# Optimization experiments

Hardware: AMD Instinct MI355X
Metric: run time of the kernel (lower is better)

## Reference

```python
import jax, jax.numpy as jnp
import numpy as np


def setup_inputs() -> dict:
    key = jax.random.key(0)
    kq, kk, kv = jax.random.split(key, 3)
    n, m, d, v = 4096, 4096, 1024, 1024
    Q = jax.random.normal(kq, (n, d), dtype=jnp.float32)
    K = jax.random.normal(kk, (m, d), dtype=jnp.float32)
    V = jax.random.normal(kv, (m, v), dtype=jnp.float32)
    return {"Q": Q, "K": K, "V": V}


def reference(Q, K, V):
    d = K.shape[-1]
    scale = d ** (-0.5)
    logits = jnp.matmul(Q, K.T)                      # [n, m]
    # Faithful to source: softmax over dim=1 (keys), THEN scaled by d**-0.5
    scores = jax.nn.softmax(logits, axis=1) * scale  # [n, m]
    return jnp.matmul(scores, V)                     # [n, v]
```

## Files before the change

kernel.cpp:

```cpp
#include <hip/hip_runtime.h>
#include <hip/hip_bf16.h>

typedef _Float16 f16x8 __attribute__((ext_vector_type(8)));
typedef _Float16 f16x4 __attribute__((ext_vector_type(4)));
typedef float f32x4 __attribute__((ext_vector_type(4)));

__device__ __forceinline__ void async_ld16(_Float16* lds, const _Float16* g) {
    __builtin_amdgcn_global_load_lds(
        (const __attribute__((address_space(1))) void*)g,
        (__attribute__((address_space(3))) void*)lds, 16, 0, 0);
}

#define VMCNT(n) asm volatile("s_waitcnt vmcnt(" #n ")" ::: "memory")
#define LGKMCNT0 asm volatile("s_waitcnt lgkmcnt(0)" ::: "memory")
#define BAR() __builtin_amdgcn_s_barrier()

template <typename CT>
__global__ __launch_bounds__(512, 2) void gemm_bt256(
    const _Float16* __restrict__ A,
    const _Float16* __restrict__ B,
    CT* __restrict__ C,
    int M, int N, int K, int Ks)
{
    __shared__ _Float16 Asm[2][256 * 64];
    __shared__ _Float16 Bsm[2][256 * 64];

    const int tid  = threadIdx.x;
    const int w    = tid >> 6;
    const int lane = tid & 63;
    const int l16  = lane & 15;
    const int quad = lane >> 4;
    const int wm   = w >> 2;
    const int wn   = w & 3;

    const int gx = gridDim.x, gy = gridDim.y;
    const int total = gx * gy * (int)gridDim.z;
    int lid = (int)blockIdx.x + gx * ((int)blockIdx.y + gy * (int)blockIdx.z);
    int bx, by, bz;
    if (gx == 16 && gy == 16 && gridDim.z == 1) {
        const int xcd = lid & 7, i = lid >> 3;
        bx = (xcd & 1) * 8 + (i & 7);
        by = (xcd >> 1) * 4 + (i >> 3);
        bz = 0;
    } else {
        const int q = total >> 3, r = total & 7;
        const int xcd = lid & 7, i = lid >> 3;
        lid = (xcd < r ? xcd * (q + 1) : r * (q + 1) + (xcd - r) * q) + i;
        bx = lid % gx;
        by = (lid / gx) % gy;
        bz = lid / (gx * gy);
    }

    const int row0 = by * 256;
    const int col0 = bx * 256;

    const _Float16* Ab = A + (size_t)row0 * K + (size_t)bz * Ks;
    const _Float16* Bb = B + (size_t)col0 * K + (size_t)bz * Ks;

    const int lr = lane >> 3;
    const int lc = (lane & 7) ^ lr;
    const size_t soff  = (size_t)(w * 16 + lr) * K + lc * 8;
    const _Float16* pa = Ab + soff;
    const _Float16* pb = Bb + soff;
    const size_t jstep = (size_t)8 * K;
    const size_t hstep = (size_t)128 * K;

    auto STAGE = [&](_Float16* sm, const _Float16* gsrc, int h, int kcol) {
        _Float16* d = sm + h * 8192 + w * 1024;
        const _Float16* s = gsrc + (size_t)h * hstep + kcol;
        async_ld16(d,       s);
        async_ld16(d + 512, s + jstep);
    };

    const int abase = (wm * 16 + l16) * 64;
    const int bbase = (wn * 16 + l16) * 64;
    const int rs0   = ((quad)     ^ (l16 & 7)) * 8;
    const int rs1   = ((4 + quad) ^ (l16 & 7)) * 8;

#define READ_A(dst, msoff)                                                     \
    _Pragma("unroll")                                                          \
    for (int m_ = 0; m_ < 4; ++m_) {                                           \
        dst[m_][0] = *(const f16x8*)(abuf + (msoff) + m_ * 2048 + abase + rs0);\
        dst[m_][1] = *(const f16x8*)(abuf + (msoff) + m_ * 2048 + abase + rs1);\
    }
#define READ_B(dst, nsoff)                                                     \
    _Pragma("unroll")                                                          \
    for (int n_ = 0; n_ < 2; ++n_) {                                           \
        dst[n_][0] = *(const f16x8*)(bbuf + (nsoff) + n_ * 4096 + bbase + rs0);\
        dst[n_][1] = *(const f16x8*)(bbuf + (nsoff) + n_ * 4096 + bbase + rs1);\
    }
#define MFMA4x2(accrow, afrag, bfrag, bcol)                                    \
    _Pragma("unroll")                                                          \
    for (int m_ = 0; m_ < 4; ++m_)                                             \
      _Pragma("unroll")                                                        \
      for (int n_ = 0; n_ < 2; ++n_) {                                         \
        acc[(accrow) + m_][(bcol) + n_] =                                      \
            __builtin_amdgcn_mfma_f32_16x16x32_f16(                            \
                afrag[m_][0], bfrag[n_][0], acc[(accrow) + m_][(bcol) + n_],   \
                0, 0, 0);                                                      \
        acc[(accrow) + m_][(bcol) + n_] =                                      \
            __builtin_amdgcn_mfma_f32_16x16x32_f16(                            \
                afrag[m_][1], bfrag[n_][1], acc[(accrow) + m_][(bcol) + n_],   \
                0, 0, 0);                                                      \
      }

    f32x4 acc[8][4] = {};
    const int NT = Ks >> 6;

    STAGE(&Asm[0][0], pa, 0, 0);
    STAGE(&Bsm[0][0], pb, 0, 0);
    STAGE(&Bsm[0][0], pb, 1, 0);
    STAGE(&Asm[0][0], pa, 1, 0);
    if (NT > 1) {
        STAGE(&Asm[1][0], pa, 0, 64);
        STAGE(&Bsm[1][0], pb, 0, 64);
        STAGE(&Bsm[1][0], pb, 1, 64);
        VMCNT(6);
    } else {
        VMCNT(0);
    }
    BAR();

    for (int t = 0; t < NT; ++t) {
        const int buf = t & 1;
        const _Float16* abuf = &Asm[buf][0];
        const _Float16* bbuf = &Bsm[buf][0];
        _Float16* const acur = &Asm[buf][0];
        _Float16* const bcur = &Bsm[buf][0];
        _Float16* const anxt = &Asm[buf ^ 1][0];

        f16x8 alo[4][2], ahi[4][2], blo[2][2], bhi[2][2];

        READ_A(alo, 0);
        READ_B(blo, 0);
        if (t + 1 < NT) STAGE(anxt, pa, 1, (t + 1) * 64);
        BAR();
        LGKMCNT0;
        __builtin_amdgcn_s_setprio(1);
        MFMA4x2(0, alo, blo, 0);
        __builtin_amdgcn_s_setprio(0);
        BAR();

        READ_B(bhi, 8192);
        if (t + 2 < NT) STAGE(acur, pa, 0, (t + 2) * 64);
        BAR();
        LGKMCNT0;
        __builtin_amdgcn_s_setprio(1);
        MFMA4x2(0, alo, bhi, 2);
        __builtin_amdgcn_s_setprio(0);
        BAR();

        READ_A(ahi, 8192);
        if (t + 2 < NT) STAGE(bcur, pb, 0, (t + 2) * 64);
        BAR();
        LGKMCNT0;
        __builtin_amdgcn_s_setprio(1);
        MFMA4x2(4, ahi, bhi, 2);
        __builtin_amdgcn_s_setprio(0);
        BAR();

        if (t + 2 < NT) STAGE(bcur, pb, 1, (t + 2) * 64);
        BAR();
        __builtin_amdgcn_s_setprio(1);
        MFMA4x2(4, ahi, blo, 0);
        __builtin_amdgcn_s_setprio(0);
        if (t + 2 < NT) { VMCNT(6); } else { VMCNT(0); }
        BAR();
    }

    CT* Cb = C + (size_t)bz * ((size_t)M * N);
    #pragma unroll
    for (int i = 0; i < 8; ++i) {
        const int ms = i >> 2, m = i & 3;
        const int gr = row0 + ms * 128 + m * 32 + wm * 16 + quad * 4;
        #pragma unroll
        for (int j = 0; j < 4; ++j) {
            const int ns = j >> 1, nn = j & 1;
            const int gc = col0 + ns * 128 + nn * 64 + wn * 16 + l16;
            const f32x4 v = acc[i][j];
            #pragma unroll
            for (int e = 0; e < 4; ++e)
                Cb[(size_t)(gr + e) * N + gc] = (CT)v[e];
        }
    }
#undef READ_A
#undef READ_B
#undef MFMA4x2
}

__global__ __launch_bounds__(256) void gemm_bt(
    const _Float16* __restrict__ A,
    const _Float16* __restrict__ B,
    float* __restrict__ C,
    int M, int N, int K, int Ks)
{
    __shared__ _Float16 At[2][128 * 32];
    __shared__ _Float16 Bt[2][128 * 32];

    const int tid  = threadIdx.x;
    const int wave = tid >> 6;
    const int lane = tid & 63;

    int gx = gridDim.x, gy = gridDim.y;
    int bx = blockIdx.x, by = blockIdx.y;
    if (((gx & 7) == 0) && ((gy & 7) == 0)) {
        const int bid    = bx + gx * by;
        const int ntx    = gx >> 3;
        const int sid    = bid >> 6;
        const int within = bid & 63;
        const int sx = sid % ntx;
        const int sy = sid / ntx;
        bx = (sx << 3) + (within & 7);
        by = (sy << 3) + (within >> 3);
    }
    const int row0 = by * 128;
    const int col0 = bx * 128;

    const int wr = (wave >> 1) * 64;
    const int wc = (wave & 1) * 64;
    const int quad = lane >> 4;
    const int l16  = lane & 15;

    f32x4 acc[4][4] = {};

    const int srow  = lane >> 2;
    const int skoff = (lane & 3) * 8;
    const size_t K64 = (size_t)64 * K;

    const _Float16* Ab = A + (size_t)row0 * K + (size_t)blockIdx.z * Ks;
    const _Float16* Bb = B + (size_t)col0 * K + (size_t)blockIdx.z * Ks;
    float* Cb = C + (size_t)blockIdx.z * M * N;

    const _Float16* pa = Ab + (size_t)(wave * 16 + srow) * K + skoff;
    const _Float16* pb = Bb + (size_t)(wave * 16 + srow) * K + skoff;

    async_ld16(At[0] + wave * 512,       pa);
    async_ld16(At[0] + (wave + 4) * 512, pa + K64);
    async_ld16(Bt[0] + wave * 512,       pb);
    async_ld16(Bt[0] + (wave + 4) * 512, pb + K64);
    __syncthreads();

    int cur = 0;
    for (int k0 = 0; k0 < Ks; k0 += 32) {
        const int nxt = cur ^ 1;
        if (k0 + 32 < Ks) {
            const _Float16* qa = pa + k0 + 32;
            const _Float16* qb = pb + k0 + 32;
            async_ld16(At[nxt] + wave * 512,       qa);
            async_ld16(At[nxt] + (wave + 4) * 512, qa + K64);
            async_ld16(Bt[nxt] + wave * 512,       qb);
            async_ld16(Bt[nxt] + (wave + 4) * 512, qb + K64);
        }

        f16x8 af[4], bf[4];
        #pragma unroll
        for (int r = 0; r < 4; ++r)
            af[r] = *(const f16x8*)&At[cur][(wr + r * 16 + l16) * 32 + quad * 8];
        #pragma unroll
        for (int c = 0; c < 4; ++c)
            bf[c] = *(const f16x8*)&Bt[cur][(wc + c * 16 + l16) * 32 + quad * 8];

        #pragma unroll
        for (int r = 0; r < 4; ++r)
            #pragma unroll
            for (int c = 0; c < 4; ++c)
                acc[r][c] = __builtin_amdgcn_mfma_f32_16x16x32_f16(af[r], bf[c], acc[r][c], 0, 0, 0);

        __syncthreads();
        cur = nxt;
    }

    #pragma unroll
    for (int r = 0; r < 4; ++r) {
        const int growb = row0 + wr + r * 16 + quad * 4;
        #pragma unroll
        for (int c = 0; c < 4; ++c) {
            const int gcol = col0 + wc + c * 16 + l16;
            #pragma unroll
            for (int i = 0; i < 4; ++i)
                Cb[(size_t)(growb + i) * N + gcol] = acc[r][c][i];
        }
    }
}

__global__ __launch_bounds__(256) void softmax_rows(
    const float* __restrict__ S, _Float16* __restrict__ P, float scale)
{
    __shared__ float red[4];
    const int row = blockIdx.x;
    const int tid = threadIdx.x;
    const int wave = tid >> 6;
    const float4* Sr = (const float4*)(S + (size_t)row * 4096);

    float4 x[4];
    #pragma unroll
    for (int i = 0; i < 4; ++i) x[i] = Sr[tid + i * 256];

    float mx = -3.402823466e+38f;
    #pragma unroll
    for (int i = 0; i < 4; ++i)
        mx = fmaxf(mx, fmaxf(fmaxf(x[i].x, x[i].y), fmaxf(x[i].z, x[i].w)));
    #pragma unroll
    for (int off = 32; off > 0; off >>= 1) mx = fmaxf(mx, __shfl_down(mx, off));
    if ((tid & 63) == 0) red[wave] = mx;
    __syncthreads();
    mx = fmaxf(fmaxf(red[0], red[1]), fmaxf(red[2], red[3]));
    __syncthreads();

    float sum = 0.0f;
    #pragma unroll
    for (int i = 0; i < 4; ++i) {
        x[i].x = __expf(x[i].x - mx);
        x[i].y = __expf(x[i].y - mx);
        x[i].z = __expf(x[i].z - mx);
        x[i].w = __expf(x[i].w - mx);
        sum += x[i].x + x[i].y + x[i].z + x[i].w;
    }
    #pragma unroll
    for (int off = 32; off > 0; off >>= 1) sum += __shfl_down(sum, off);
    if ((tid & 63) == 0) red[wave] = sum;
    __syncthreads();
    sum = red[0] + red[1] + red[2] + red[3];

    const float inv = scale / sum;
    f16x4* Pr = (f16x4*)(P + (size_t)row * 4096);
    #pragma unroll
    for (int i = 0; i < 4; ++i) {
        f16x4 h;
        h.x = (_Float16)(x[i].x * inv);
        h.y = (_Float16)(x[i].y * inv);
        h.z = (_Float16)(x[i].z * inv);
        h.w = (_Float16)(x[i].w * inv);
        Pr[tid + i * 256] = h;
    }
}

__global__ __launch_bounds__(256) void prep(
    const float4* __restrict__ Qs, f16x4* __restrict__ Qh, int n4q,
    const float4* __restrict__ Ks, f16x4* __restrict__ Kh, int n4k,
    const float* __restrict__ V, _Float16* __restrict__ Vt, int rows, int cols)
{
    __shared__ float tile[32][33];
    if (blockIdx.y == 0) {
        int i = blockIdx.x * 256 + threadIdx.x;
        const int stride = gridDim.x * 256;
        const int tot = n4q + n4k;
        for (; i < tot; i += stride) {
            const float4* s = (i < n4q) ? (Qs + i) : (Ks + (i - n4q));
            f16x4* dst = (i < n4q) ? (Qh + i) : (Kh + (i - n4q));
            float4 v = *s;
            f16x4 h;
            h.x = (_Float16)v.x; h.y = (_Float16)v.y;
            h.z = (_Float16)v.z; h.w = (_Float16)v.w;
            *dst = h;
        }
    } else {
        const int cb = blockIdx.x & 31;
        const int rb = blockIdx.x >> 5;
        const int c0 = cb * 32;
        const int r0 = rb * 32;
        const int tx = threadIdx.x & 31;
        const int ty = threadIdx.x >> 5;
        #pragma unroll
        for (int i = 0; i < 4; ++i)
            tile[ty * 4 + i][tx] = V[(size_t)(r0 + ty * 4 + i) * cols + c0 + tx];
        __syncthreads();
        #pragma unroll
        for (int i = 0; i < 4; ++i)
            Vt[(size_t)(c0 + ty * 4 + i) * rows + r0 + tx] = (_Float16)tile[tx][ty * 4 + i];
    }
}

__global__ __launch_bounds__(256) void cvt2_f32_f16(
    const float4* __restrict__ a, f16x4* __restrict__ da, int n4a,
    const float4* __restrict__ b, f16x4* __restrict__ db, int n4b)
{
    int i = blockIdx.x * 256 + threadIdx.x;
    const int stride = gridDim.x * 256;
    const int tot = n4a + n4b;
    for (; i < tot; i += stride) {
        const float4* s = (i < n4a) ? (a + i) : (b + (i - n4a));
        f16x4* d = (i < n4a) ? (da + i) : (db + (i - n4a));
        float4 v = *s;
        f16x4 h;
        h.x = (_Float16)v.x; h.y = (_Float16)v.y;
        h.z = (_Float16)v.z; h.w = (_Float16)v.w;
        *d = h;
    }
}

__global__ __launch_bounds__(256) void transpose_cvt(
    const float* __restrict__ V, _Float16* __restrict__ Vt, int rows, int cols)
{
    __shared__ float tile[32][33];
    const int c0 = blockIdx.x * 32;
    const int r0 = blockIdx.y * 32;
    const int tx = threadIdx.x & 31;
    const int ty = threadIdx.x >> 5;
    #pragma unroll
    for (int i = 0; i < 4; ++i)
        tile[ty * 4 + i][tx] = V[(size_t)(r0 + ty * 4 + i) * cols + c0 + tx];
    __syncthreads();
    #pragma unroll
    for (int i = 0; i < 4; ++i)
        Vt[(size_t)(c0 + ty * 4 + i) * rows + r0 + tx] = (_Float16)tile[tx][ty * 4 + i];
}

__global__ __launch_bounds__(256) void reduce2(
    const float4* __restrict__ a, const float4* __restrict__ b,
    float4* __restrict__ o, int n4)
{
    int i = blockIdx.x * 256 + threadIdx.x;
    const int stride = gridDim.x * 256;
    for (; i < n4; i += stride) {
        float4 u = a[i], v = b[i];
        float4 w;
        w.x = u.x + v.x; w.y = u.y + v.y; w.z = u.z + v.z; w.w = u.w + v.w;
        o[i] = w;
    }
}

__global__ __launch_bounds__(256) void reduce4h(
    const f16x8* __restrict__ a, const f16x8* __restrict__ b,
    const f16x8* __restrict__ c, const f16x8* __restrict__ d,
    float4* __restrict__ o, int n8)
{
    int i = blockIdx.x * 256 + threadIdx.x;
    const int stride = gridDim.x * 256;
    for (; i < n8; i += stride) {
        f16x8 u = a[i], v = b[i], x = c[i], y = d[i];
        float s[8];
        #pragma unroll
        for (int e = 0; e < 8; ++e)
            s[e] = ((float)u[e] + (float)v[e]) + ((float)x[e] + (float)y[e]);
        float4 o0, o1;
        o0.x = s[0]; o0.y = s[1]; o0.z = s[2]; o0.w = s[3];
        o1.x = s[4]; o1.y = s[5]; o1.z = s[6]; o1.w = s[7];
        o[2 * i]     = o0;
        o[2 * i + 1] = o1;
    }
}

extern "C" void kernel_launch(void* const* d_in, const int* in_sizes, int n_in,
                              void* d_out, int out_size, void* d_ws, size_t ws_size,
                              hipStream_t stream) {
    const float* Q = (const float*)d_in[0];
    const float* K = (const float*)d_in[1];
    const float* V = (const float*)d_in[2];
    float* out = (float*)d_out;

    const int n = 4096, m = 4096, d = 1024, vdim = 1024;
    const float scale = 0.03125f;

    char* w = (char*)d_ws;
    _Float16* Qh = (_Float16*)w;
    _Float16* Kh = (_Float16*)(w + (8u << 20));
    _Float16* Vt = (_Float16*)(w + (16u << 20));
    char* rest = w + (24u << 20);
    size_t avail = ws_size > (24u << 20) ? ws_size - (24u << 20) : 0;

    int nc = 128;
    if      ((size_t)4096 * m * 6 <= avail) nc = 4096;
    else if ((size_t)2048 * m * 6 <= avail) nc = 2048;
    else if ((size_t)1024 * m * 6 <= avail) nc = 1024;
    else if ((size_t)512  * m * 6 <= avail) nc = 512;
    else if ((size_t)256  * m * 6 <= avail) nc = 256;

    float*    S = (float*)rest;
    _Float16* P = (_Float16*)(rest + (size_t)nc * m * 4);
    _Float16* partH = (_Float16*)rest;

    if (nc >= 256) {
        prep<<<dim3(4096, 2), dim3(256), 0, stream>>>(
            (const float4*)Q, (f16x4*)Qh, n * d / 4,
            (const float4*)K, (f16x4*)Kh, m * d / 4,
            V, Vt, m, vdim);
        for (int r0 = 0; r0 < n; r0 += nc) {
            gemm_bt256<float><<<dim3(m / 256, nc / 256, 1), dim3(512), 0, stream>>>(
                Qh + (size_t)r0 * d, Kh, S, nc, m, d, d);
            softmax_rows<<<dim3(nc), dim3(256), 0, stream>>>(S, P, scale);
            gemm_bt256<_Float16><<<dim3(vdim / 256, nc / 256, 4), dim3(512), 0, stream>>>(
                P, Vt, partH, nc, vdim, m, m / 4);
            reduce4h<<<dim3(1024), dim3(256), 0, stream>>>(
                (const f16x8*)partH,
                (const f16x8*)(partH + (size_t)nc * vdim),
                (const f16x8*)(partH + (size_t)2 * nc * vdim),
                (const f16x8*)(partH + (size_t)3 * nc * vdim),
                (float4*)(out + (size_t)r0 * vdim), nc * vdim / 8);
        }
    } else {
        float* part = S;
        cvt2_f32_f16<<<dim3(2048), dim3(256), 0, stream>>>(
            (const float4*)Q, (f16x4*)Qh, n * d / 4,
            (const float4*)K, (f16x4*)Kh, m * d / 4);
        transpose_cvt<<<dim3(vdim / 32, m / 32), dim3(256), 0, stream>>>(V, Vt, m, vdim);
        for (int r0 = 0; r0 < n; r0 += nc) {
            gemm_bt<<<dim3(m / 128, nc / 128, 1), dim3(256), 0, stream>>>(
                Qh + (size_t)r0 * d, Kh, S, nc, m, d, d);
            softmax_rows<<<dim3(nc), dim3(256), 0, stream>>>(S, P, scale);
            gemm_bt<<<dim3(vdim / 128, nc / 128, 2), dim3(256), 0, stream>>>(
                P, Vt, part, nc, vdim, m, m / 2);
            reduce2<<<dim3(1024), dim3(256), 0, stream>>>(
                (const float4*)part, (const float4*)(part + (size_t)nc * vdim),
                (float4*)(out + (size_t)r0 * vdim), nc * vdim / 4);
        }
    }
}
```

Measured before the change: 189.6 us.

## Fuse attention pipeline into one persistent cooperative kernel with grid syncs

Replaces the five separate launches (prep, QK gemm, softmax, PV gemm, reduce) with a single cooperative kernel of 256 blocks that runs each stage in turn, separated by grid.sync. The GEMM body is factored into a device function so both kernels share it. The aim is to remove launch gaps and tail effects between stages. In exchange it adds grid-wide barrier cost and fixes occupancy at 256 blocks for the conversion and softmax stages, with a fallback to the old path if the cooperative launch fails.

```diff
diff --git a/kernel.cpp b/kernel.cpp
--- a/kernel.cpp
+++ b/kernel.cpp
@@ -1,5 +1,8 @@
 #include <hip/hip_runtime.h>
 #include <hip/hip_bf16.h>
+#include <hip/hip_cooperative_groups.h>
+
+namespace cg = cooperative_groups;
 
 typedef _Float16 f16x8 __attribute__((ext_vector_type(8)));
 typedef _Float16 f16x4 __attribute__((ext_vector_type(4)));
@@ -16,15 +19,14 @@
 #define BAR() __builtin_amdgcn_s_barrier()
 
 template <typename CT>
-__global__ __launch_bounds__(512, 2) void gemm_bt256(
+__device__ __forceinline__ void gemm_body(
+    _Float16* __restrict__ AsmP, _Float16* __restrict__ BsmP,
     const _Float16* __restrict__ A,
     const _Float16* __restrict__ B,
     CT* __restrict__ C,
-    int M, int N, int K, int Ks)
-{
-    __shared__ _Float16 Asm[2][256 * 64];
-    __shared__ _Float16 Bsm[2][256 * 64];
-
+    int M, int N, int K, int Ks,
+    int bx, int by, int bz)
+{
     const int tid  = threadIdx.x;
     const int w    = tid >> 6;
     const int lane = tid & 63;
@@ -32,6 +34,153 @@
     const int quad = lane >> 4;
     const int wm   = w >> 2;
     const int wn   = w & 3;
+
+    const int row0 = by * 256;
+    const int col0 = bx * 256;
+
+    const _Float16* Ab = A + (size_t)row0 * K + (size_t)bz * Ks;
+    const _Float16* Bb = B + (size_t)col0 * K + (size_t)bz * Ks;
+
+    const int lr = lane >> 3;
+    const int lc = (lane & 7) ^ lr;
+    const size_t soff  = (size_t)(w * 16 + lr) * K + lc * 8;
+    const _Float16* pa = Ab + soff;
+    const _Float16* pb = Bb + soff;
+    const size_t jstep = (size_t)8 * K;
+    const size_t hstep = (size_t)128 * K;
+
+    auto STAGE = [&](_Float16* sm, const _Float16* gsrc, int h, int kcol) {
+        _Float16* d = sm + h * 8192 + w * 1024;
+        const _Float16* s = gsrc + (size_t)h * hstep + kcol;
+        async_ld16(d,       s);
+        async_ld16(d + 512, s + jstep);
+    };
+
+    const int abase = (wm * 16 + l16) * 64;
+    const int bbase = (wn * 16 + l16) * 64;
+    const int rs0   = ((quad)     ^ (l16 & 7)) * 8;
+    const int rs1   = ((4 + quad) ^ (l16 & 7)) * 8;
+
+#define READ_A(dst, msoff)                                                     \
+    _Pragma("unroll")                                                          \
+    for (int m_ = 0; m_ < 4; ++m_) {                                           \
+        dst[m_][0] = *(const f16x8*)(abuf + (msoff) + m_ * 2048 + abase + rs0);\
+        dst[m_][1] = *(const f16x8*)(abuf + (msoff) + m_ * 2048 + abase + rs1);\
+    }
+#define READ_B(dst, nsoff)                                                     \
+    _Pragma("unroll")                                                          \
+    for (int n_ = 0; n_ < 2; ++n_) {                                           \
+        dst[n_][0] = *(const f16x8*)(bbuf + (nsoff) + n_ * 4096 + bbase + rs0);\
+        dst[n_][1] = *(const f16x8*)(bbuf + (nsoff) + n_ * 4096 + bbase + rs1);\
+    }
+#define MFMA4x2(accrow, afrag, bfrag, bcol)                                    \
+    _Pragma("unroll")                                                          \
+    for (int m_ = 0; m_ < 4; ++m_)                                             \
+      _Pragma("unroll")                                                        \
+      for (int n_ = 0; n_ < 2; ++n_) {                                         \
+        acc[(accrow) + m_][(bcol) + n_] =                                      \
+            __builtin_amdgcn_mfma_f32_16x16x32_f16(                            \
+                afrag[m_][0], bfrag[n_][0], acc[(accrow) + m_][(bcol) + n_],   \
+                0, 0, 0);                                                      \
+        acc[(accrow) + m_][(bcol) + n_] =                                      \
+            __builtin_amdgcn_mfma_f32_16x16x32_f16(                            \
+                afrag[m_][1], bfrag[n_][1], acc[(accrow) + m_][(bcol) + n_],   \
+                0, 0, 0);                                                      \
+      }
+
+    f32x4 acc[8][4] = {};
+    const int NT = Ks >> 6;
+
+    STAGE(AsmP, pa, 0, 0);
+    STAGE(BsmP, pb, 0, 0);
+    STAGE(BsmP, pb, 1, 0);
+    STAGE(AsmP, pa, 1, 0);
+    if (NT > 1) {
+        STAGE(AsmP + 16384, pa, 0, 64);
+        STAGE(BsmP + 16384, pb, 0, 64);
+        STAGE(BsmP + 16384, pb, 1, 64);
+        VMCNT(6);
+    } else {
+        VMCNT(0);
+    }
+    BAR();
+
+    for (int t = 0; t < NT; ++t) {
+        const int buf = t & 1;
+        const _Float16* abuf = AsmP + buf * 16384;
+        const _Float16* bbuf = BsmP + buf * 16384;
+        _Float16* const acur = AsmP + buf * 16384;
+        _Float16* const bcur = BsmP + buf * 16384;
+        _Float16* const anxt = AsmP + (buf ^ 1) * 16384;
+
+        f16x8 alo[4][2], ahi[4][2], blo[2][2], bhi[2][2];
+
+        READ_A(alo, 0);
+        READ_B(blo, 0);
+        if (t + 1 < NT) STAGE(anxt, pa, 1, (t + 1) * 64);
+        BAR();
+        LGKMCNT0;
+        __builtin_amdgcn_s_setprio(1);
+        MFMA4x2(0, alo, blo, 0);
+        __builtin_amdgcn_s_setprio(0);
+        BAR();
+
+        READ_B(bhi, 8192);
+        if (t + 2 < NT) STAGE(acur, pa, 0, (t + 2) * 64);
+        BAR();
+        LGKMCNT0;
+        __builtin_amdgcn_s_setprio(1);
+        MFMA4x2(0, alo, bhi, 2);
+        __builtin_amdgcn_s_setprio(0);
+        BAR();
+
+        READ_A(ahi, 8192);
+        if (t + 2 < NT) STAGE(bcur, pb, 0, (t + 2) * 64);
+        BAR();
+        LGKMCNT0;
+        __builtin_amdgcn_s_setprio(1);
+        MFMA4x2(4, ahi, bhi, 2);
+        __builtin_amdgcn_s_setprio(0);
+        BAR();
+
+        if (t + 2 < NT) STAGE(bcur, pb, 1, (t + 2) * 64);
+        BAR();
+        __builtin_amdgcn_s_setprio(1);
+        MFMA4x2(4, ahi, blo, 0);
+        __builtin_amdgcn_s_setprio(0);
+        if (t + 2 < NT) { VMCNT(6); } else { VMCNT(0); }
+        BAR();
+    }
+
+    CT* Cb = C + (size_t)bz * ((size_t)M * N);
+    #pragma unroll
+    for (int i = 0; i < 8; ++i) {
+        const int ms = i >> 2, m = i & 3;
+        const int gr = row0 + ms * 128 + m * 32 + wm * 16 + quad * 4;
+        #pragma unroll
+        for (int j = 0; j < 4; ++j) {
+            const int ns = j >> 1, nn = j & 1;
+            const int gc = col0 + ns * 128 + nn * 64 + wn * 16 + l16;
+            const f32x4 v = acc[i][j];
+            #pragma unroll
+            for (int e = 0; e < 4; ++e)
+                Cb[(size_t)(gr + e) * N + gc] = (CT)v[e];
+        }
+    }
+#undef READ_A
+#undef READ_B
+#undef MFMA4x2
+}
+
+template <typename CT>
+__global__ __launch_bounds__(512, 2) void gemm_bt256(
+    const _Float16* __restrict__ A,
+    const _Float16* __restrict__ B,
+    CT* __restrict__ C,
+    int M, int N, int K, int Ks)
+{
+    __shared__ _Float16 Asm[2 * 256 * 64];
+    __shared__ _Float16 Bsm[2 * 256 * 64];
 
     const int gx = gridDim.x, gy = gridDim.y;
     const int total = gx * gy * (int)gridDim.z;
@@ -50,142 +199,148 @@
         by = (lid / gx) % gy;
         bz = lid / (gx * gy);
     }
-
-    const int row0 = by * 256;
-    const int col0 = bx * 256;
-
-    const _Float16* Ab = A + (size_t)row0 * K + (size_t)bz * Ks;
-    const _Float16* Bb = B + (size_t)col0 * K + (size_t)bz * Ks;
-
-    const int lr = lane >> 3;
-    const int lc = (lane & 7) ^ lr;
-    const size_t soff  = (size_t)(w * 16 + lr) * K + lc * 8;
-    const _Float16* pa = Ab + soff;
-    const _Float16* pb = Bb + soff;
-    const size_t jstep = (size_t)8 * K;
-    const size_t hstep = (size_t)128 * K;
-
-    auto STAGE = [&](_Float16* sm, const _Float16* gsrc, int h, int kcol) {
-        _Float16* d = sm + h * 8192 + w * 1024;
-        const _Float16* s = gsrc + (size_t)h * hstep + kcol;
-        async_ld16(d,       s);
-        async_ld16(d + 512, s + jstep);
-    };
-
-    const int abase = (wm * 16 + l16) * 64;
-    const int bbase = (wn * 16 + l16) * 64;
-    const int rs0   = ((quad)     ^ (l16 & 7)) * 8;
-    const int rs1   = ((4 + quad) ^ (l16 & 7)) * 8;
-
-#define READ_A(dst, msoff)                                                     \
-    _Pragma("unroll")                                                          \
-    for (int m_ = 0; m_ < 4; ++m_) {                                           \
-        dst[m_][0] = *(const f16x8*)(abuf + (msoff) + m_ * 2048 + abase + rs0);\
-        dst[m_][1] = *(const f16x8*)(abuf + (msoff) + m_ * 2048 + abase + rs1);\
-    }
-#define READ_B(dst, nsoff)                                                     \
-    _Pragma("unroll")                                                          \
-    for (int n_ = 0; n_ < 2; ++n_) {                                           \
-        dst[n_][0] = *(const f16x8*)(bbuf + (nsoff) + n_ * 4096 + bbase + rs0);\
-        dst[n_][1] = *(const f16x8*)(bbuf + (nsoff) + n_ * 4096 + bbase + rs1);\
-    }
-#define MFMA4x2(accrow, afrag, bfrag, bcol)                                    \
-    _Pragma("unroll")                                                          \
-    for (int m_ = 0; m_ < 4; ++m_)                                             \
-      _Pragma("unroll")                                                        \
-      for (int n_ = 0; n_ < 2; ++n_) {                                         \
-        acc[(accrow) + m_][(bcol) + n_] =                                      \
-            __builtin_amdgcn_mfma_f32_16x16x32_f16(                            \
-                afrag[m_][0], bfrag[n_][0], acc[(accrow) + m_][(bcol) + n_],   \
-                0, 0, 0);                                                      \
-        acc[(accrow) + m_][(bcol) + n_] =                                      \
-            __builtin_amdgcn_mfma_f32_16x16x32_f16(                            \
-                afrag[m_][1], bfrag[n_][1], acc[(accrow) + m_][(bcol) + n_],   \
-                0, 0, 0);                                                      \
-      }
-
-    f32x4 acc[8][4] = {};
-    const int NT = Ks >> 6;
-
-    STAGE(&Asm[0][0], pa, 0, 0);
-    STAGE(&Bsm[0][0], pb, 0, 0);
-    STAGE(&Bsm[0][0], pb, 1, 0);
-    STAGE(&Asm[0][0], pa, 1, 0);
-    if (NT > 1) {
-        STAGE(&Asm[1][0], pa, 0, 64);
-        STAGE(&Bsm[1][0], pb, 0, 64);
-        STAGE(&Bsm[1][0], pb, 1, 64);
-        VMCNT(6);
-    } else {
-        VMCNT(0);
-    }
-    BAR();
-
-    for (int t = 0; t < NT; ++t) {
-        const int buf = t & 1;
-        const _Float16* abuf = &Asm[buf][0];
-        const _Float16* bbuf = &Bsm[buf][0];
-        _Float16* const acur = &Asm[buf][0];
-        _Float16* const bcur = &Bsm[buf][0];
-        _Float16* const anxt = &Asm[buf ^ 1][0];
-
-        f16x8 alo[4][2], ahi[4][2], blo[2][2], bhi[2][2];
-
-        READ_A(alo, 0);
-        READ_B(blo, 0);
-        if (t + 1 < NT) STAGE(anxt, pa, 1, (t + 1) * 64);
-        BAR();
-        LGKMCNT0;
-        __builtin_amdgcn_s_setprio(1);
-        MFMA4x2(0, alo, blo, 0);
-        __builtin_amdgcn_s_setprio(0);
-        BAR();
-
-        READ_B(bhi, 8192);
-        if (t + 2 < NT) STAGE(acur, pa, 0, (t + 2) * 64);
-        BAR();
-        LGKMCNT0;
-        __builtin_amdgcn_s_setprio(1);
-        MFMA4x2(0, alo, bhi, 2);
-        __builtin_amdgcn_s_setprio(0);
-        BAR();
-
-        READ_A(ahi, 8192);
-        if (t + 2 < NT) STAGE(bcur, pb, 0, (t + 2) * 64);
-        BAR();
-        LGKMCNT0;
-        __builtin_amdgcn_s_setprio(1);
-        MFMA4x2(4, ahi, bhi, 2);
-        __builtin_amdgcn_s_setprio(0);
-        BAR();
-
-        if (t + 2 < NT) STAGE(bcur, pb, 1, (t + 2) * 64);
-        BAR();
-        __builtin_amdgcn_s_setprio(1);
-        MFMA4x2(4, ahi, blo, 0);
-        __builtin_amdgcn_s_setprio(0);
-        if (t + 2 < NT) { VMCNT(6); } else { VMCNT(0); }
-        BAR();
-    }
-
-    CT* Cb = C + (size_t)bz * ((size_t)M * N);
-    #pragma unroll
-    for (int i = 0; i < 8; ++i) {
-        const int ms = i >> 2, m = i & 3;
-        const int gr = row0 + ms * 128 + m * 32 + wm * 16 + quad * 4;
-        #pragma unroll
-        for (int j = 0; j < 4; ++j) {
-            const int ns = j >> 1, nn = j & 1;
-            const int gc = col0 + ns * 128 + nn * 64 + wn * 16 + l16;
-            const f32x4 v = acc[i][j];
-            #pragma unroll
-            for (int e = 0; e < 4; ++e)
-                Cb[(size_t)(gr + e) * N + gc] = (CT)v[e];
-        }
-    }
-#undef READ_A
-#undef READ_B
-#undef MFMA4x2
+    gemm_body<CT>(Asm, Bsm, A, B, C, M, N, K, Ks, bx, by, bz);
+}
+
+__global__ __launch_bounds__(512, 2) void fused_attn(
+    const float* __restrict__ Q, const float* __restrict__ K,
+    const float* __restrict__ V,
+    _Float16* __restrict__ Qh, _Float16* __restrict__ Kh,
+    _Float16* __restrict__ Vt,
+    float* __restrict__ S, _Float16* __restrict__ P,
+    _Float16* __restrict__ partH, float* __restrict__ out,
+    float scale)
+{
+    __shared__ _Float16 Asm[2 * 256 * 64];
+    __shared__ _Float16 Bsm[2 * 256 * 64];
+    __shared__ float red8[8];
+
+    const int bid = blockIdx.x;
+    const int tid = threadIdx.x;
+    cg::grid_group grid = cg::this_grid();
+
+    {
+        const int tot4 = (4096 * 1024 / 4) * 2;
+        for (int i = bid * 512 + tid; i < tot4; i += 256 * 512) {
+            const bool isQ = i < tot4 / 2;
+            const float4* s = isQ ? ((const float4*)Q + i)
+                                  : ((const float4*)K + (i - tot4 / 2));
+            f16x4* dst = isQ ? ((f16x4*)Qh + i) : ((f16x4*)Kh + (i - tot4 / 2));
+            float4 v = *s;
+            f16x4 h;
+            h.x = (_Float16)v.x; h.y = (_Float16)v.y;
+            h.z = (_Float16)v.z; h.w = (_Float16)v.w;
+            *dst = h;
+        }
+        const int h  = tid >> 8;
+        const int ts = tid & 255;
+        const int tx = ts & 31;
+        const int ty = ts >> 5;
+        float* tile = (float*)&Asm[0] + h * (32 * 33);
+        for (int tIdx = bid * 2 + h; tIdx < 4096; tIdx += 512) {
+            const int rb = tIdx >> 5;
+            const int cb = tIdx & 31;
+            const int r0 = rb * 32, c0 = cb * 32;
+            #pragma unroll
+            for (int i = 0; i < 4; ++i)
+                tile[(ty * 4 + i) * 33 + tx] =
+                    V[(size_t)(r0 + ty * 4 + i) * 1024 + c0 + tx];
+            __syncthreads();
+            #pragma unroll
+            for (int i = 0; i < 4; ++i)
+                Vt[(size_t)(c0 + ty * 4 + i) * 4096 + r0 + tx] =
+                    (_Float16)tile[tx * 33 + ty * 4 + i];
+            __syncthreads();
+        }
+    }
+    __threadfence();
+    grid.sync();
+
+    {
+        const int xcd = bid & 7, i = bid >> 3;
+        const int bx = (xcd & 1) * 8 + (i & 7);
+        const int by = (xcd >> 1) * 4 + (i >> 3);
+        gemm_body<float>(Asm, Bsm, Qh, Kh, S, 4096, 4096, 1024, 1024, bx, by, 0);
+    }
+    __threadfence();
+    grid.sync();
+
+    {
+        const int wv = tid >> 6, ln = tid & 63;
+        for (int rr = 0; rr < 16; ++rr) {
+            const int r = bid * 16 + rr;
+            const float4* Sr = (const float4*)(S + (size_t)r * 4096);
+            const float4 x0 = Sr[tid * 2];
+            const float4 x1 = Sr[tid * 2 + 1];
+            float mx = fmaxf(fmaxf(fmaxf(x0.x, x0.y), fmaxf(x0.z, x0.w)),
+                             fmaxf(fmaxf(x1.x, x1.y), fmaxf(x1.z, x1.w)));
+            #pragma unroll
+            for (int off = 32; off > 0; off >>= 1)
+                mx = fmaxf(mx, __shfl_down(mx, off));
+            if (ln == 0) red8[wv] = mx;
+            __syncthreads();
+            mx = red8[0];
+            #pragma unroll
+            for (int q2 = 1; q2 < 8; ++q2) mx = fmaxf(mx, red8[q2]);
+            __syncthreads();
+
+            float e0 = __expf(x0.x - mx), e1 = __expf(x0.y - mx);
+            float e2 = __expf(x0.z - mx), e3 = __expf(x0.w - mx);
+            float e4 = __expf(x1.x - mx), e5 = __expf(x1.y - mx);
+            float e6 = __expf(x1.z - mx), e7 = __expf(x1.w - mx);
+            float sum = ((e0 + e1) + (e2 + e3)) + ((e4 + e5) + (e6 + e7));
+            #pragma unroll
+            for (int off = 32; off > 0; off >>= 1)
+                sum += __shfl_down(sum, off);
+            if (ln == 0) red8[wv] = sum;
+            __syncthreads();
+            sum = ((red8[0] + red8[1]) + (red8[2] + red8[3])) +
+                  ((red8[4] + red8[5]) + (red8[6] + red8[7]));
+            __syncthreads();
+
+            const float inv = scale / sum;
+            f16x8 h;
+            h[0] = (_Float16)(e0 * inv); h[1] = (_Float16)(e1 * inv);
+            h[2] = (_Float16)(e2 * inv); h[3] = (_Float16)(e3 * inv);
+            h[4] = (_Float16)(e4 * inv); h[5] = (_Float16)(e5 * inv);
+            h[6] = (_Float16)(e6 * inv); h[7] = (_Float16)(e7 * inv);
+            ((f16x8*)(P + (size_t)r * 4096))[tid] = h;
+        }
+    }
+    __threadfence();
+    grid.sync();
+
+    {
+        const int xcd = bid & 7, i = bid >> 3;
+        const int lid2 = xcd * 32 + i;
+        const int bx = lid2 & 3;
+        const int by = (lid2 >> 2) & 15;
+        const int bz = lid2 >> 6;
+        gemm_body<_Float16>(Asm, Bsm, P, Vt, partH, 4096, 1024, 4096, 1024,
+                            bx, by, bz);
+    }
+    __threadfence();
+    grid.sync();
+
+    {
+        const f16x8* a  = (const f16x8*)partH;
+        const f16x8* b2 = a + 524288;
+        const f16x8* c2 = a + 2 * 524288;
+        const f16x8* d2 = a + 3 * 524288;
+        float4* o = (float4*)out;
+        for (int i = bid * 512 + tid; i < 524288; i += 256 * 512) {
+            f16x8 u = a[i], v = b2[i], x = c2[i], y = d2[i];
+            float s[8];
+            #pragma unroll
+            for (int e = 0; e < 8; ++e)
+                s[e] = ((float)u[e] + (float)v[e]) + ((float)x[e] + (float)y[e]);
+            float4 o0, o1;
+            o0.x = s[0]; o0.y = s[1]; o0.z = s[2]; o0.w = s[3];
+            o1.x = s[4]; o1.y = s[5]; o1.z = s[6]; o1.w = s[7];
+            o[2 * i]     = o0;
+            o[2 * i + 1] = o1;
+        }
+    }
 }
 
 __global__ __launch_bounds__(256) void gemm_bt(
@@ -470,7 +625,22 @@
     _Float16* P = (_Float16*)(rest + (size_t)nc * m * 4);
     _Float16* partH = (_Float16*)rest;
 
-    if (nc >= 256) {
+    bool done = false;
+    if (nc == 4096) {
+        const float* Qp = Q; const float* Kp = K; const float* Vp = V;
+        _Float16* QhP = Qh; _Float16* KhP = Kh; _Float16* VtP = Vt;
+        float* SP = S; _Float16* PP = P; _Float16* pHP = partH;
+        float* outP = out; float scl = scale;
+        void* args[] = {(void*)&Qp, (void*)&Kp, (void*)&Vp,
+                        (void*)&QhP, (void*)&KhP, (void*)&VtP,
+                        (void*)&SP, (void*)&PP, (void*)&pHP,
+                        (void*)&outP, (void*)&scl};
+        hipError_t e = hipLaunchCooperativeKernel(
+            (const void*)fused_attn, dim3(256), dim3(512), args, 0, stream);
+        done = (e == hipSuccess);
+    }
+
+    if (!done && nc >= 256) {
         prep<<<dim3(4096, 2), dim3(256), 0, stream>>>(
             (const float4*)Q, (f16x4*)Qh, n * d / 4,
             (const float4*)K, (f16x4*)Kh, m * d / 4,
@@ -488,7 +658,7 @@
                 (const f16x8*)(partH + (size_t)3 * nc * vdim),
                 (float4*)(out + (size_t)r0 * vdim), nc * vdim / 8);
         }
-    } else {
+    } else if (!done) {
         float* part = S;
         cvt2_f32_f16<<<dim3(2048), dim3(256), 0, stream>>>(
             (const float4*)Q, (f16x4*)Qh, n * d / 4,
```

After: 556.6 us. +193.6%, slower.
